# Performance work log

Hardware: AMD Instinct MI355X
Metric: run time of the kernel (lower is better)

Reference implementation:

```python
import jax, jax.numpy as jnp
import numpy as np

NUM_HEADS = 8
ALPHA = 4.0
BN_EPS = 1e-5


def _dwconv(x, w, pad):
    # x: [B, C, H, W], w: [C, 1, kh, kw] depthwise (groups == C)
    return jax.lax.conv_general_dilated(
        x, w, window_strides=(1, 1), padding=[(pad, pad), (pad, pad)],
        dimension_numbers=('NCHW', 'OIHW', 'NCHW'),
        feature_group_count=x.shape[1])


def _forward(x, qg_w, kv_w, proj_w, proj_b, dwc_w, dwc_b, power_p, scale_p,
             enh_w, bn_gamma, bn_beta, enhance_weight, pos_enc):
    B, N, C = x.shape
    H = W = int(round(N ** 0.5))
    h = NUM_HEADS
    d = C // h

    # qg linear (no bias): [B, N, 2C] -> q, g
    qg = jnp.einsum('bnc,oc->bno', x, qg_w)
    q, g = qg[..., :C], qg[..., C:]

    # SpatialFilterEnhancer on q: depthwise 3x3 conv + BN(train) + ReLU
    qi = q.transpose(0, 2, 1).reshape(B, C, H, W)
    qe = _dwconv(qi, enh_w, pad=1)
    m = qe.mean(axis=(0, 2, 3), keepdims=True)
    var = qe.var(axis=(0, 2, 3), keepdims=True)
    qe = (qe - m) * jax.lax.rsqrt(var + BN_EPS)
    qe = qe * bn_gamma[None, :, None, None] + bn_beta[None, :, None, None]
    qe = jax.nn.relu(qe)
    q_enh = qe.reshape(B, C, N).transpose(0, 2, 1)
    q = q + enhance_weight * q_enh

    # kv linear (sr_ratio == 1 path)
    kv = jnp.einsum('bnc,oc->bno', x, kv_w)
    k, v = kv[..., :C], kv[..., C:]
    k = k + pos_enc  # learned positional encoding, shape [1, N, C]
    n = k.shape[1]

    scale = jax.nn.softplus(scale_p)              # [1, 1, C]
    power = 1.0 + ALPHA * jax.nn.sigmoid(power_p)  # [1, h, 1, d]
    q = q / scale
    k = k / scale

    # split heads: [B, h, N, d]
    q = q.reshape(B, N, h, d).transpose(0, 2, 1, 3)
    k = k.reshape(B, n, h, d).transpose(0, 2, 1, 3)
    v = v.reshape(B, n, h, d).transpose(0, 2, 1, 3)

    # power-law kernel feature maps
    q_pos = jax.nn.relu(q) ** power
    q_neg = jax.nn.relu(-q) ** power
    k_pos = jax.nn.relu(k) ** power
    k_neg = jax.nn.relu(-k) ** power
    q_sim = jnp.concatenate([q_pos, q_neg], axis=-1)   # [B, h, N, 2d]
    q_opp = jnp.concatenate([q_neg, q_pos], axis=-1)
    kf = jnp.concatenate([k_pos, k_neg], axis=-1)      # [B, h, n, 2d]
    v1, v2 = jnp.split(v, 2, axis=-1)                  # [B, h, n, d/2] each

    k_mean = kf.mean(axis=-2)  # [B, h, 2d]
    inv_n = 1.0 / n

    # sim branch
    z = 1.0 / (jnp.einsum('bhnd,bhd->bhn', q_sim, k_mean)[..., None] + 1e-6)
    kv1 = jnp.einsum('bhnd,bhne->bhde', kf, v1) * inv_n  # (n^-0.5)*(n^-0.5)
    x_sim = jnp.einsum('bhnd,bhde->bhne', q_sim, kv1) * z

    # opp branch
    z2 = 1.0 / (jnp.einsum('bhnd,bhd->bhn', q_opp, k_mean)[..., None] + 1e-6)
    kv2 = jnp.einsum('bhnd,bhne->bhde', kf, v2) * inv_n
    x_opp = jnp.einsum('bhnd,bhde->bhne', q_opp, kv2) * z2

    xa = jnp.concatenate([x_sim, x_opp], axis=-1)       # [B, h, N, d]
    xa = xa.transpose(0, 2, 1, 3).reshape(B, N, C)

    # depthwise conv positional branch on v (sr_ratio == 1 -> no interpolate)
    vimg = v.reshape(B * h, H, W, d).transpose(0, 3, 1, 2)  # [B*h, d, H, W]
    vd = _dwconv(vimg, dwc_w, pad=2) + dwc_b[None, :, None, None]
    v_out = vd.reshape(B, C, N).transpose(0, 2, 1)          # [B, N, C]

    out = (xa + v_out) * g
    out = jnp.einsum('bnc,oc->bno', out, proj_w) + proj_b
    return out


def setup_inputs() -> dict:
    key = jax.random.key(0)
    ks = jax.random.split(key, 10)
    B, N, C = 8, 3136, 512
    h = NUM_HEADS
    d = C // h
    f = lambda k, shape, s=0.02: jax.random.normal(k, shape, jnp.float32) * s
    return dict(
        x=jax.random.normal(ks[0], (B, N, C), jnp.float32),
        qg_w=f(ks[1], (2 * C, C)),
        kv_w=f(ks[2], (2 * C, C)),
        proj_w=f(ks[3], (C, C)),
        proj_b=jnp.zeros((C,), jnp.float32),
        dwc_w=f(ks[4], (d, 1, 5, 5), 0.1),
        dwc_b=jnp.zeros((d,), jnp.float32),
        power_p=f(ks[5], (1, h, 1, d), 0.1),
        scale_p=f(ks[6], (1, 1, C), 0.1),
        enh_w=f(ks[7], (C, 1, 3, 3), 0.1),
        bn_gamma=jnp.ones((C,), jnp.float32),
        bn_beta=jnp.zeros((C,), jnp.float32),
        enhance_weight=jnp.float32(0.5),
        pos_enc=f(ks[8], (1, N, C)),
    )


def reference(x, qg_w, kv_w, proj_w, proj_b, dwc_w, dwc_b, power_p, scale_p,
              enh_w, bn_gamma, bn_beta, enhance_weight, pos_enc):
    return _forward(x, qg_w, kv_w, proj_w, proj_b, dwc_w, dwc_b, power_p,
                    scale_p, enh_w, bn_gamma, bn_beta, enhance_weight, pos_enc)
```

## Files before the change

### kernel.cpp

```cpp
#include <hip/hip_runtime.h>
#include <hip/hip_bf16.h>
#include <math.h>

#define CDIM 512
#define NTOK 3136
#define BATCH 8
#define MTOT (BATCH*NTOK)
#define NHEAD 8
#define DHEAD 64
#define HW 56

typedef __attribute__((ext_vector_type(8))) short short8;
typedef __attribute__((ext_vector_type(4))) float f32x4;

__device__ __forceinline__ ushort f2bf(float f) {
    union { float f; unsigned int u; } v; v.f = f;
    unsigned int u = v.u + 0x7FFFu + ((v.u >> 16) & 1u);
    return (ushort)(u >> 16);
}
__device__ __forceinline__ float bf2f(ushort u) {
    union { unsigned int u; float f; } v; v.u = ((unsigned int)u) << 16;
    return v.f;
}

__device__ __forceinline__ void gload_lds16(const void* g, void* lds) {
    __builtin_amdgcn_global_load_lds((const __attribute__((address_space(1))) void*)g,
                                     (__attribute__((address_space(3))) void*)lds,
                                     16, 0, 0);
}

__global__ void prep_kernel(const float* __restrict__ scale_p,
                            const float* __restrict__ power_p,
                            float* __restrict__ inv_scale,
                            float* __restrict__ power) {
    int c = threadIdx.x;
    if (c < CDIM) {
        float s = log1pf(expf(scale_p[c]));
        inv_scale[c] = 1.0f / s;
        power[c] = 1.0f + 4.0f / (1.0f + expf(-power_p[c]));
    }
}

__global__ __launch_bounds__(256) void cvt_bf16_kernel(const float* __restrict__ src,
                                                       ushort* __restrict__ dst, int n4) {
    int i = blockIdx.x * 256 + threadIdx.x;
    if (i < n4) {
        float4 f = ((const float4*)src)[i];
        ushort4 o;
        o.x = f2bf(f.x); o.y = f2bf(f.y); o.z = f2bf(f.z); o.w = f2bf(f.w);
        ((ushort4*)dst)[i] = o;
    }
}

__global__ __launch_bounds__(256) void mgemm_qgkv(const ushort* __restrict__ A,
                                                  const ushort* __restrict__ Wqg,
                                                  const ushort* __restrict__ Wkv,
                                                  ushort* __restrict__ Qout,
                                                  ushort* __restrict__ Gout,
                                                  ushort* __restrict__ KFout,
                                                  ushort* __restrict__ Vout,
                                                  const float* __restrict__ pos,
                                                  const float* __restrict__ invs,
                                                  const float* __restrict__ powr) {
    __shared__ __align__(16) char smem[65536];
    ushort* At = (ushort*)smem;
    ushort* Bt = (ushort*)(smem + 32768);
    float*  Osh = (float*)smem;

    const int t = threadIdx.x;
    const int w = t >> 6, l = t & 63;
    const int wr = w >> 1, wc = w & 1;
    const int r8 = l >> 3, sl = l & 7;
    const int ss = sl ^ r8;

    const int bid = blockIdx.x;
    const int idp = (bid & 7) * 392 + (bid >> 3);
    const int mb = idp >> 4, ob = idp & 15;
    const int m0 = mb * 128;
    const ushort* Bp = (ob < 8) ? (Wqg + (size_t)ob * 128 * CDIM)
                                : (Wkv + (size_t)(ob - 8) * 128 * CDIM);

    auto stage = [&](int buf, int ks) {
        const int k0 = ks * 64;
        #pragma unroll
        for (int c = 0; c < 4; ++c) {
            int rc = (w * 4 + c) * 8 + r8;
            gload_lds16(A + (size_t)(m0 + rc) * CDIM + k0 + ss * 8, At + buf * 8192 + (w * 4 + c) * 512);
            gload_lds16(Bp + (size_t)rc * CDIM + k0 + ss * 8, Bt + buf * 8192 + (w * 4 + c) * 512);
        }
    };

    f32x4 acc[4][4] = {};
    stage(0, 0);
    __syncthreads();
    for (int ks = 0; ks < 8; ++ks) {
        int cur = ks & 1;
        if (ks < 7) stage(cur ^ 1, ks + 1);
        #pragma unroll
        for (int kk = 0; kk < 2; ++kk) {
            short8 af[4], bfr[4];
            const int sbase = kk * 4 + (l >> 4);
            #pragma unroll
            for (int i = 0; i < 4; ++i) {
                int row = wr * 64 + i * 16 + (l & 15);
                af[i] = *(const short8*)&At[cur * 8192 + row * 64 + ((sbase ^ (row & 7)) * 8)];
                int rowb = wc * 64 + i * 16 + (l & 15);
                bfr[i] = *(const short8*)&Bt[cur * 8192 + rowb * 64 + ((sbase ^ (rowb & 7)) * 8)];
            }
            #pragma unroll
            for (int i = 0; i < 4; ++i)
                #pragma unroll
                for (int j = 0; j < 4; ++j)
                    acc[i][j] = __builtin_amdgcn_mfma_f32_16x16x32_bf16(af[i], bfr[j], acc[i][j], 0, 0, 0);
        }
        __syncthreads();
    }

    #pragma unroll
    for (int i = 0; i < 4; ++i)
        #pragma unroll
        for (int j = 0; j < 4; ++j)
            #pragma unroll
            for (int rr = 0; rr < 4; ++rr) {
                int row = wr * 64 + i * 16 + (l >> 4) * 4 + rr;
                int col = wc * 64 + j * 16 + (l & 15);
                int pc = col ^ (((row >> 2) & 1) << 4);
                Osh[row * 128 + pc] = acc[i][j][rr];
            }
    __syncthreads();

    const int colbase = ob * 128;
    #pragma unroll
    for (int q = 0; q < 16; ++q) {
        int fi = q * 256 + t;
        int r = fi >> 5, c4 = (fi & 31) * 4;
        int pc4 = c4 ^ (((r >> 2) & 1) << 4);
        float4 v = *(float4*)&Osh[r * 128 + pc4];
        int m = m0 + r;
        if (colbase < 512) {
            ushort4 o;
            o.x = f2bf(v.x); o.y = f2bf(v.y); o.z = f2bf(v.z); o.w = f2bf(v.w);
            *(ushort4*)&Qout[(size_t)m * CDIM + colbase + c4] = o;
        } else if (colbase < 1024) {
            ushort4 o;
            o.x = f2bf(v.x); o.y = f2bf(v.y); o.z = f2bf(v.z); o.w = f2bf(v.w);
            *(ushort4*)&Gout[(size_t)m * CDIM + colbase - 512 + c4] = o;
        } else if (colbase < 1536) {
            int n = m % NTOK;
            int oc = colbase - 1024 + c4;
            float4 pv = *(const float4*)&pos[(size_t)n * CDIM + oc];
            float4 iv = *(const float4*)&invs[oc];
            float4 pw = *(const float4*)&powr[oc];
            float kx0 = (v.x + pv.x) * iv.x, kx1 = (v.y + pv.y) * iv.y;
            float kx2 = (v.z + pv.z) * iv.z, kx3 = (v.w + pv.w) * iv.w;
            float t0 = __powf(fabsf(kx0), pw.x), t1 = __powf(fabsf(kx1), pw.y);
            float t2 = __powf(fabsf(kx2), pw.z), t3 = __powf(fabsf(kx3), pw.w);
            ushort4 up, un;
            up.x = kx0 > 0.f ? f2bf(t0) : 0; un.x = kx0 < 0.f ? f2bf(t0) : 0;
            up.y = kx1 > 0.f ? f2bf(t1) : 0; un.y = kx1 < 0.f ? f2bf(t1) : 0;
            up.z = kx2 > 0.f ? f2bf(t2) : 0; un.z = kx2 < 0.f ? f2bf(t2) : 0;
            up.w = kx3 > 0.f ? f2bf(t3) : 0; un.w = kx3 < 0.f ? f2bf(t3) : 0;
            ushort* dst = KFout + (size_t)m * 1024 + ((oc >> 6) << 7) + (oc & 63);
            *(ushort4*)dst = up;
            *(ushort4*)(dst + 64) = un;
        } else {
            ushort4 o;
            o.x = f2bf(v.x); o.y = f2bf(v.y); o.z = f2bf(v.z); o.w = f2bf(v.w);
            *(ushort4*)&Vout[(size_t)m * CDIM + colbase - 1536 + c4] = o;
        }
    }
}

__global__ __launch_bounds__(256) void mgemm_proj(const ushort* __restrict__ A,
                                                  const ushort* __restrict__ W,
                                                  float* __restrict__ out,
                                                  const float* __restrict__ pb) {
    __shared__ __align__(16) char smem[65536];
    ushort* At = (ushort*)smem;
    ushort* Bt = (ushort*)(smem + 32768);
    float*  Osh = (float*)smem;

    const int t = threadIdx.x;
    const int w = t >> 6, l = t & 63;
    const int wr = w >> 1, wc = w & 1;
    const int r8 = l >> 3, sl = l & 7;
    const int ss = sl ^ r8;

    const int bid = blockIdx.x;
    const int idp = (bid & 7) * 98 + (bid >> 3);
    const int mb = idp >> 2, ob = idp & 3;
    const int m0 = mb * 128;
    const ushort* Bp = W + (size_t)ob * 128 * CDIM;

    auto stage = [&](int buf, int ks) {
        const int k0 = ks * 64;
        #pragma unroll
        for (int c = 0; c < 4; ++c) {
            int rc = (w * 4 + c) * 8 + r8;
            gload_lds16(A + (size_t)(m0 + rc) * CDIM + k0 + ss * 8, At + buf * 8192 + (w * 4 + c) * 512);
            gload_lds16(Bp + (size_t)rc * CDIM + k0 + ss * 8, Bt + buf * 8192 + (w * 4 + c) * 512);
        }
    };

    f32x4 acc[4][4] = {};
    stage(0, 0);
    __syncthreads();
    for (int ks = 0; ks < 8; ++ks) {
        int cur = ks & 1;
        if (ks < 7) stage(cur ^ 1, ks + 1);
        #pragma unroll
        for (int kk = 0; kk < 2; ++kk) {
            short8 af[4], bfr[4];
            const int sbase = kk * 4 + (l >> 4);
            #pragma unroll
            for (int i = 0; i < 4; ++i) {
                int row = wr * 64 + i * 16 + (l & 15);
                af[i] = *(const short8*)&At[cur * 8192 + row * 64 + ((sbase ^ (row & 7)) * 8)];
                int rowb = wc * 64 + i * 16 + (l & 15);
                bfr[i] = *(const short8*)&Bt[cur * 8192 + rowb * 64 + ((sbase ^ (rowb & 7)) * 8)];
            }
            #pragma unroll
            for (int i = 0; i < 4; ++i)
                #pragma unroll
                for (int j = 0; j < 4; ++j)
                    acc[i][j] = __builtin_amdgcn_mfma_f32_16x16x32_bf16(af[i], bfr[j], acc[i][j], 0, 0, 0);
        }
        __syncthreads();
    }

    #pragma unroll
    for (int i = 0; i < 4; ++i)
        #pragma unroll
        for (int j = 0; j < 4; ++j)
            #pragma unroll
            for (int rr = 0; rr < 4; ++rr) {
                int row = wr * 64 + i * 16 + (l >> 4) * 4 + rr;
                int col = wc * 64 + j * 16 + (l & 15);
                int pc = col ^ (((row >> 2) & 1) << 4);
                Osh[row * 128 + pc] = acc[i][j][rr];
            }
    __syncthreads();

    const int colbase = ob * 128;
    #pragma unroll
    for (int q = 0; q < 16; ++q) {
        int fi = q * 256 + t;
        int r = fi >> 5, c4 = (fi & 31) * 4;
        int pc4 = c4 ^ (((r >> 2) & 1) << 4);
        float4 v = *(float4*)&Osh[r * 128 + pc4];
        float4 b4 = *(const float4*)&pb[colbase + c4];
        v.x += b4.x; v.y += b4.y; v.z += b4.z; v.w += b4.w;
        *(float4*)&out[(size_t)(m0 + r) * CDIM + colbase + c4] = v;
    }
}

__global__ __launch_bounds__(256) void conv3s_kernel(const ushort* __restrict__ Qbf,
                                                     const float* __restrict__ enh_w,
                                                     ushort* __restrict__ QEbf,
                                                     float* __restrict__ ssum,
                                                     float* __restrict__ ssq) {
    const int t = threadIdx.x;
    const int c0 = t * 2;
    const int xpos = blockIdx.x;
    const int byc = blockIdx.y;
    const int b = byc >> 2, yc = byc & 3;
    const int y0 = yc * 14;

    float wgt[9][2];
    #pragma unroll
    for (int tap = 0; tap < 9; ++tap) {
        wgt[tap][0] = enh_w[c0 * 9 + tap];
        wgt[tap][1] = enh_w[(c0 + 1) * 9 + tap];
    }
    const size_t base = (size_t)b * NTOK * CDIM + c0;

    float2 win[3][3];
    auto ldrow = [&](int yy, float2* dst) {
        #pragma unroll
        for (int dx = 0; dx < 3; ++dx) {
            int xx = xpos + dx - 1;
            bool ok = (yy >= 0 && yy < HW && xx >= 0 && xx < HW);
            if (ok) {
                ushort2 uv = *(const ushort2*)(Qbf + base + ((size_t)(yy * HW + xx) << 9));
                dst[dx] = make_float2(bf2f(uv.x), bf2f(uv.y));
            } else {
                dst[dx] = make_float2(0.f, 0.f);
            }
        }
    };
    ldrow(y0 - 1, win[0]);
    ldrow(y0,     win[1]);

    float s1a = 0.f, s2a = 0.f, s1b = 0.f, s2b = 0.f;
    #pragma unroll
    for (int i = 0; i < 14; ++i) {
        int y = y0 + i;
        ldrow(y + 1, win[(i + 2) % 3]);
        float a0 = 0.f, a1 = 0.f;
        #pragma unroll
        for (int dy = 0; dy < 3; ++dy) {
            float2* row = win[(i + dy) % 3];
            #pragma unroll
            for (int dx = 0; dx < 3; ++dx) {
                a0 = fmaf(row[dx].x, wgt[dy * 3 + dx][0], a0);
                a1 = fmaf(row[dx].y, wgt[dy * 3 + dx][1], a1);
            }
        }
        ushort2 o; o.x = f2bf(a0); o.y = f2bf(a1);
        *(ushort2*)(QEbf + base + ((size_t)(y * HW + xpos) << 9)) = o;
        s1a += a0; s2a += a0 * a0;
        s1b += a1; s2b += a1 * a1;
    }
    atomicAdd(&ssum[c0], s1a);     atomicAdd(&ssq[c0], s2a);
    atomicAdd(&ssum[c0 + 1], s1b); atomicAdd(&ssq[c0 + 1], s2b);
}

__global__ void bnprep_kernel(const float* __restrict__ ssum, const float* __restrict__ ssq,
                              const float* __restrict__ bn_g, const float* __restrict__ bn_b,
                              float* __restrict__ achan, float* __restrict__ bchan) {
    int c = threadIdx.x;
    if (c < CDIM) {
        const float invM = 1.0f / (float)MTOT;
        float mean = ssum[c] * invM;
        float var  = ssq[c] * invM - mean * mean;
        float a = bn_g[c] * rsqrtf(var + 1e-5f);
        achan[c] = a;
        bchan[c] = bn_b[c] - mean * a;
    }
}

__global__ __launch_bounds__(256) void kvred4_kernel(const ushort* __restrict__ KF,
                                                     const ushort* __restrict__ Vbf,
                                                     float* __restrict__ PKV) {
    const int bh = blockIdx.x, chunk = blockIdx.y;
    const int b = bh >> 3, head = bh & 7;
    const int t = threadIdx.x;
    const int w = t >> 6, l = t & 63;
    const int lr = l & 15;
    const int ns = (l >> 4) * 8;

    const int nbase = b * NTOK + chunk * 448;
    const ushort* kf0 = KF  + ((size_t)(nbase + ns)) * 1024 + head * 128 + (w * 32 + lr);
    const ushort* vb0 = Vbf + ((size_t)(nbase + ns)) * 512  + head * 64  + lr;

    short8 ones;
    #pragma unroll
    for (int j = 0; j < 8; ++j) ones[j] = (lr == 0) ? (short)0x3F80 : (short)0;

    f32x4 acc[2][5] = {};
    for (int tile = 0; tile < 14; ++tile) {
        union { uint u[4]; short8 s; } ua[2], ub[4];
        #pragma unroll
        for (int i = 0; i < 2; ++i) {
            #pragma unroll
            for (int j = 0; j < 4; ++j) {
                uint lo = kf0[i * 16 + (size_t)(2 * j) * 1024];
                uint hi = kf0[i * 16 + (size_t)(2 * j + 1) * 1024];
                ua[i].u[j] = lo | (hi << 16);
            }
        }
        #pragma unroll
        for (int j5 = 0; j5 < 4; ++j5) {
            #pragma unroll
            for (int j = 0; j < 4; ++j) {
                uint lo = vb0[j5 * 16 + (size_t)(2 * j) * 512];
                uint hi = vb0[j5 * 16 + (size_t)(2 * j + 1) * 512];
                ub[j5].u[j] = lo | (hi << 16);
            }
        }
        #pragma unroll
        for (int i = 0; i < 2; ++i) {
            #pragma unroll
            for (int j5 = 0; j5 < 4; ++j5)
                acc[i][j5] = __builtin_amdgcn_mfma_f32_16x16x32_bf16(ua[i].s, ub[j5].s, acc[i][j5], 0, 0, 0);
            acc[i][4] = __builtin_amdgcn_mfma_f32_16x16x32_bf16(ua[i].s, ones, acc[i][4], 0, 0, 0);
        }
        kf0 += (size_t)32 * 1024;
        vb0 += (size_t)32 * 512;
    }
    size_t base = ((size_t)(chunk * 64 + bh)) * 8320;
    #pragma unroll
    for (int i = 0; i < 2; ++i) {
        int d0 = w * 32 + i * 16 + (l >> 4) * 4;
        #pragma unroll
        for (int j = 0; j < 5; ++j) {
            int e = j * 16 + lr;
            if (j < 4 || e == 64)
                *(f32x4*)(PKV + base + (size_t)e * 128 + d0) = acc[i][j];
        }
    }
}

__global__ __launch_bounds__(256) void kvreduce2_kernel(const float* __restrict__ PKV,
                                                        ushort* __restrict__ kvTbf) {
    int gid = blockIdx.x * 256 + threadIdx.x;
    const float inv_n = 1.0f / (float)NTOK;
    int bh = gid / 10240;
    int r  = gid - bh * 10240;
    int row = r >> 7, dcol = r & 127;
    int dlog = (((dcol >> 3) ^ (row & 7)) << 3) | (dcol & 7);
    float s = 0.f;
    if (row < 64) {
        int dsel = (row >= 32) ? (dlog ^ 64) : dlog;
        #pragma unroll
        for (int c = 0; c < 7; ++c) s += PKV[(size_t)c * 532480 + (size_t)bh * 8320 + row * 128 + dsel];
    } else if (row < 66) {
        int dsel = (row == 65) ? (dlog ^ 64) : dlog;
        #pragma unroll
        for (int c = 0; c < 7; ++c) s += PKV[(size_t)c * 532480 + (size_t)bh * 8320 + 64 * 128 + dsel];
    }
    kvTbf[gid] = (row < 66) ? f2bf(s * inv_n) : (ushort)0;
}

__global__ __launch_bounds__(256) void attn_mfma_kernel(const ushort* __restrict__ Qbf,
                                                        const ushort* __restrict__ QEbf,
                                                        const ushort* __restrict__ kvTbf,
                                                        const float* __restrict__ power,
                                                        const float* __restrict__ achan,
                                                        const float* __restrict__ bchan,
                                                        const float* __restrict__ invs,
                                                        const float* __restrict__ ewp,
                                                        ushort* __restrict__ ATTbf) {
    __shared__ ushort QF[64 * 128];
    __shared__ ushort BT[80 * 128];
    const int bh = blockIdx.x, tb = blockIdx.y;
    const int b = bh >> 3, head = bh & 7;
    const int t = threadIdx.x;
    const int w = t >> 6, l = t & 63;

    #pragma unroll
    for (int i = 0; i < 5; ++i) {
        int f = i * 256 + t;
        gload_lds16(kvTbf + (size_t)bh * 10240 + f * 8, BT + f * 8);
    }

    const int c = l, hc = head * 64 + c;
    const float p = power[hc];
    const float ac = achan[hc], bc = bchan[hc], iv = invs[hc], ew = ewp[0];
    #pragma unroll
    for (int i = 0; i < 16; ++i) {
        int tok = i * 4 + w;
        size_t off = ((size_t)(b * NTOK + tb * 64 + tok)) * CDIM + hc;
        float q = bf2f(Qbf[off]);
        float qe = bf2f(QEbf[off]);
        q = (q + ew * fmaxf(fmaf(ac, qe, bc), 0.f)) * iv;
        float ax = fabsf(q);
        float tp = ax > 0.f ? __powf(ax, p) : 0.f;
        float qp = q > 0.f ? tp : 0.f;
        float qn = q < 0.f ? tp : 0.f;
        int sw = tok & 7;
        QF[tok * 128 + (((c >> 3) ^ sw) * 8) + (c & 7)]       = f2bf(qp);
        QF[tok * 128 + ((((c >> 3) + 8) ^ sw) * 8) + (c & 7)] = f2bf(qn);
    }
    __syncthreads();

    f32x4 acc[5] = {};
    #pragma unroll
    for (int kk = 0; kk < 4; ++kk) {
        int sbase = kk * 4 + (l >> 4);
        int rowa = w * 16 + (l & 15);
        short8 af = *(const short8*)&QF[rowa * 128 + ((sbase ^ (rowa & 7)) * 8)];
        #pragma unroll
        for (int j = 0; j < 5; ++j) {
            int rowb = j * 16 + (l & 15);
            short8 bf = *(const short8*)&BT[rowb * 128 + ((sbase ^ (rowb & 7)) * 8)];
            acc[j] = __builtin_amdgcn_mfma_f32_16x16x32_bf16(af, bf, acc[j], 0, 0, 0);
        }
    }
    __syncthreads();

    ushort* Oout = QF;
    #pragma unroll
    for (int rr = 0; rr < 4; ++rr) {
        float ssim = __shfl(acc[4][rr], (l & 48));
        float sopp = __shfl(acc[4][rr], (l & 48) + 1);
        float zs = 1.f / (ssim + 1e-6f);
        float zo = 1.f / (sopp + 1e-6f);
        int tokl = w * 16 + (l >> 4) * 4 + rr;
        #pragma unroll
        for (int j = 0; j < 4; ++j) {
            int e = j * 16 + (l & 15);
            Oout[tokl * 64 + e] = f2bf(acc[j][rr] * (j < 2 ? zs : zo));
        }
    }
    __syncthreads();

    #pragma unroll
    for (int i = 0; i < 2; ++i) {
        int idx = i * 256 + t;
        int tokl = idx >> 3, ch = (idx & 7) * 8;
        short8 vv = *(short8*)&Oout[tokl * 64 + ch];
        *(short8*)&ATTbf[((size_t)(b * NTOK + tb * 64 + tokl)) * CDIM + head * 64 + ch] = vv;
    }
}

__global__ __launch_bounds__(256) void voutg2_kernel(const ushort* __restrict__ Vbf,
                                                     const ushort* __restrict__ ATTbf,
                                                     const ushort* __restrict__ Gbf,
                                                     const float* __restrict__ dwc_w,
                                                     const float* __restrict__ dwc_b,
                                                     ushort* __restrict__ PRE) {
    const int t = threadIdx.x;
    const int c0 = t * 2;
    const int xpos = blockIdx.x;
    const int byc = blockIdx.y;
    const int b = byc >> 2, yc = byc & 3;
    const int y0 = yc * 14;
    const int dch = c0 & 63;

    float wgt[25][2];
    #pragma unroll
    for (int tap = 0; tap < 25; ++tap) {
        wgt[tap][0] = dwc_w[dch * 25 + tap];
        wgt[tap][1] = dwc_w[(dch + 1) * 25 + tap];
    }
    const float bias0 = dwc_b[dch], bias1 = dwc_b[dch + 1];
    const size_t base = (size_t)b * NTOK * CDIM + c0;

    float2 win[5][5];
    auto ldrow = [&](int yy, float2* dst) {
        #pragma unroll
        for (int dx = 0; dx < 5; ++dx) {
            int xx = xpos + dx - 2;
            bool ok = (yy >= 0 && yy < HW && xx >= 0 && xx < HW);
            if (ok) {
                ushort2 uv = *(const ushort2*)(Vbf + base + ((size_t)(yy * HW + xx) << 9));
                dst[dx] = make_float2(bf2f(uv.x), bf2f(uv.y));
            } else {
                dst[dx] = make_float2(0.f, 0.f);
            }
        }
    };
    ldrow(y0 - 2, win[0]);
    ldrow(y0 - 1, win[1]);
    ldrow(y0,     win[2]);
    ldrow(y0 + 1, win[3]);

    #pragma unroll
    for (int i = 0; i < 14; ++i) {
        int y = y0 + i;
        ldrow(y + 2, win[(i + 4) % 5]);
        float a0 = bias0, a1 = bias1;
        #pragma unroll
        for (int dy = 0; dy < 5; ++dy) {
            float2* row = win[(i + dy) % 5];
            #pragma unroll
            for (int dx = 0; dx < 5; ++dx) {
                a0 = fmaf(row[dx].x, wgt[dy * 5 + dx][0], a0);
                a1 = fmaf(row[dx].y, wgt[dy * 5 + dx][1], a1);
            }
        }
        size_t oidx = base + ((size_t)(y * HW + xpos) << 9);
        ushort2 au = *(const ushort2*)(ATTbf + oidx);
        ushort2 gu = *(const ushort2*)(Gbf + oidx);
        ushort2 o;
        o.x = f2bf((bf2f(au.x) + a0) * bf2f(gu.x));
        o.y = f2bf((bf2f(au.y) + a1) * bf2f(gu.y));
        *(ushort2*)(PRE + oidx) = o;
    }
}

extern "C" void kernel_launch(void* const* d_in, const int* in_sizes, int n_in,
                              void* d_out, int out_size, void* d_ws, size_t ws_size,
                              hipStream_t stream) {
    const float* x      = (const float*)d_in[0];
    const float* qg_w   = (const float*)d_in[1];
    const float* kv_w   = (const float*)d_in[2];
    const float* proj_w = (const float*)d_in[3];
    const float* proj_b = (const float*)d_in[4];
    const float* dwc_w  = (const float*)d_in[5];
    const float* dwc_b  = (const float*)d_in[6];
    const float* power_p= (const float*)d_in[7];
    const float* scale_p= (const float*)d_in[8];
    const float* enh_w  = (const float*)d_in[9];
    const float* bn_g   = (const float*)d_in[10];
    const float* bn_b   = (const float*)d_in[11];
    const float* ew_p   = (const float*)d_in[12];
    const float* pos    = (const float*)d_in[13];

    const size_t NELEM = (size_t)MTOT * CDIM;
    float* ws    = (float*)d_ws;
    ushort* Qbf  = (ushort*)ws;
    ushort* Gbf  = (ushort*)(ws + NELEM);
    float*  PKV  = ws + NELEM + NELEM / 2;
    ushort* KFbf = (ushort*)(ws + 2 * NELEM);
    ushort* PREbf= (ushort*)(ws + 2 * NELEM);
    ushort* Vbf  = (ushort*)(ws + 3 * NELEM);
    ushort* ATTbf= (ushort*)(ws + 3 * NELEM + NELEM / 2);
    ushort* Xbf  = (ushort*)(ws + 4 * NELEM);
    ushort* QEbf = (ushort*)(ws + 4 * NELEM);
    float* SMALL = ws + 5 * NELEM;
    float* ssum  = SMALL;
    float* ssq   = SMALL + 512;
    ushort* kvTbf= (ushort*)(SMALL + 9216);
    float* invs  = SMALL + 533504;
    float* powr  = SMALL + 534016;
    float* achan = SMALL + 534528;
    float* bchan = SMALL + 535040;
    ushort* Wqg  = (ushort*)(SMALL + 535552);
    ushort* Wkv  = (ushort*)(SMALL + 797696);
    ushort* Wproj= (ushort*)(SMALL + 1059840);

    hipMemsetAsync(SMALL, 0, (size_t)1024 * sizeof(float), stream);

    prep_kernel<<<1, 512, 0, stream>>>(scale_p, power_p, invs, powr);

    cvt_bf16_kernel<<<12544, 256, 0, stream>>>(x, Xbf, 3211264);
    cvt_bf16_kernel<<<512, 256, 0, stream>>>(qg_w, Wqg, 131072);
    cvt_bf16_kernel<<<512, 256, 0, stream>>>(kv_w, Wkv, 131072);
    cvt_bf16_kernel<<<256, 256, 0, stream>>>(proj_w, Wproj, 65536);

    mgemm_qgkv<<<3136, 256, 0, stream>>>(Xbf, Wqg, Wkv, Qbf, Gbf, KFbf, Vbf, pos, invs, powr);

    dim3 cgrid(56, 32);
    conv3s_kernel<<<cgrid, 256, 0, stream>>>(Qbf, enh_w, QEbf, ssum, ssq);
    bnprep_kernel<<<1, 512, 0, stream>>>(ssum, ssq, bn_g, bn_b, achan, bchan);

    kvred4_kernel<<<dim3(64, 7), 256, 0, stream>>>(KFbf, Vbf, PKV);
    kvreduce2_kernel<<<2560, 256, 0, stream>>>(PKV, kvTbf);

    attn_mfma_kernel<<<dim3(64, 49), 256, 0, stream>>>(Qbf, QEbf, kvTbf, powr,
                                                       achan, bchan, invs, ew_p, ATTbf);

    voutg2_kernel<<<cgrid, 256, 0, stream>>>(Vbf, ATTbf, Gbf, dwc_w, dwc_b, PREbf);

    mgemm_proj<<<784, 256, 0, stream>>>(PREbf, Wproj, (float*)d_out, proj_b);
}
```

Before: 502.2 us.

## Halve GEMM LDS by single-buffering tiles and staging epilogue in halves

Both bf16 GEMM kernels (qgkv and proj) drop from 64KB to 32KB of shared memory. The double-buffered K-stage pipeline becomes a single buffer with load-then-sync each step, and the output tile is written through LDS in two 64-row halves. The intent is to fit more workgroups per CU and raise occupancy. The cost is that global loads no longer overlap MFMA compute, and the epilogue gains extra barriers.

New measurement: 523.3 us. 1.04x slower.

```diff
diff --git a/kernel.cpp b/kernel.cpp
--- a/kernel.cpp
+++ b/kernel.cpp
@@ -62,9 +62,9 @@
                                                   const float* __restrict__ pos,
                                                   const float* __restrict__ invs,
                                                   const float* __restrict__ powr) {
-    __shared__ __align__(16) char smem[65536];
+    __shared__ __align__(16) char smem[32768];
     ushort* At = (ushort*)smem;
-    ushort* Bt = (ushort*)(smem + 32768);
+    ushort* Bt = (ushort*)(smem + 16384);
     float*  Osh = (float*)smem;
 
     const int t = threadIdx.x;
@@ -80,22 +80,20 @@
     const ushort* Bp = (ob < 8) ? (Wqg + (size_t)ob * 128 * CDIM)
                                 : (Wkv + (size_t)(ob - 8) * 128 * CDIM);
 
-    auto stage = [&](int buf, int ks) {
+    auto stage = [&](int ks) {
         const int k0 = ks * 64;
         #pragma unroll
         for (int c = 0; c < 4; ++c) {
             int rc = (w * 4 + c) * 8 + r8;
-            gload_lds16(A + (size_t)(m0 + rc) * CDIM + k0 + ss * 8, At + buf * 8192 + (w * 4 + c) * 512);
-            gload_lds16(Bp + (size_t)rc * CDIM + k0 + ss * 8, Bt + buf * 8192 + (w * 4 + c) * 512);
+            gload_lds16(A + (size_t)(m0 + rc) * CDIM + k0 + ss * 8, At + (w * 4 + c) * 512);
+            gload_lds16(Bp + (size_t)rc * CDIM + k0 + ss * 8, Bt + (w * 4 + c) * 512);
         }
     };
 
     f32x4 acc[4][4] = {};
-    stage(0, 0);
-    __syncthreads();
     for (int ks = 0; ks < 8; ++ks) {
-        int cur = ks & 1;
-        if (ks < 7) stage(cur ^ 1, ks + 1);
+        stage(ks);
+        __syncthreads();
         #pragma unroll
         for (int kk = 0; kk < 2; ++kk) {
             short8 af[4], bfr[4];
@@ -103,9 +101,9 @@
             #pragma unroll
             for (int i = 0; i < 4; ++i) {
                 int row = wr * 64 + i * 16 + (l & 15);
-                af[i] = *(const short8*)&At[cur * 8192 + row * 64 + ((sbase ^ (row & 7)) * 8)];
+                af[i] = *(const short8*)&At[row * 64 + ((sbase ^ (row & 7)) * 8)];
                 int rowb = wc * 64 + i * 16 + (l & 15);
-                bfr[i] = *(const short8*)&Bt[cur * 8192 + rowb * 64 + ((sbase ^ (rowb & 7)) * 8)];
+                bfr[i] = *(const short8*)&Bt[rowb * 64 + ((sbase ^ (rowb & 7)) * 8)];
             }
             #pragma unroll
             for (int i = 0; i < 4; ++i)
@@ -116,58 +114,63 @@
         __syncthreads();
     }
 
-    #pragma unroll
-    for (int i = 0; i < 4; ++i)
-        #pragma unroll
-        for (int j = 0; j < 4; ++j)
-            #pragma unroll
-            for (int rr = 0; rr < 4; ++rr) {
-                int row = wr * 64 + i * 16 + (l >> 4) * 4 + rr;
-                int col = wc * 64 + j * 16 + (l & 15);
-                int pc = col ^ (((row >> 2) & 1) << 4);
-                Osh[row * 128 + pc] = acc[i][j][rr];
-            }
-    __syncthreads();
-
     const int colbase = ob * 128;
     #pragma unroll
-    for (int q = 0; q < 16; ++q) {
-        int fi = q * 256 + t;
-        int r = fi >> 5, c4 = (fi & 31) * 4;
-        int pc4 = c4 ^ (((r >> 2) & 1) << 4);
-        float4 v = *(float4*)&Osh[r * 128 + pc4];
-        int m = m0 + r;
-        if (colbase < 512) {
-            ushort4 o;
-            o.x = f2bf(v.x); o.y = f2bf(v.y); o.z = f2bf(v.z); o.w = f2bf(v.w);
-            *(ushort4*)&Qout[(size_t)m * CDIM + colbase + c4] = o;
-        } else if (colbase < 1024) {
-            ushort4 o;
-            o.x = f2bf(v.x); o.y = f2bf(v.y); o.z = f2bf(v.z); o.w = f2bf(v.w);
-            *(ushort4*)&Gout[(size_t)m * CDIM + colbase - 512 + c4] = o;
-        } else if (colbase < 1536) {
-            int n = m % NTOK;
-            int oc = colbase - 1024 + c4;
-            float4 pv = *(const float4*)&pos[(size_t)n * CDIM + oc];
-            float4 iv = *(const float4*)&invs[oc];
-            float4 pw = *(const float4*)&powr[oc];
-            float kx0 = (v.x + pv.x) * iv.x, kx1 = (v.y + pv.y) * iv.y;
-            float kx2 = (v.z + pv.z) * iv.z, kx3 = (v.w + pv.w) * iv.w;
-            float t0 = __powf(fabsf(kx0), pw.x), t1 = __powf(fabsf(kx1), pw.y);
-            float t2 = __powf(fabsf(kx2), pw.z), t3 = __powf(fabsf(kx3), pw.w);
-            ushort4 up, un;
-            up.x = kx0 > 0.f ? f2bf(t0) : 0; un.x = kx0 < 0.f ? f2bf(t0) : 0;
-            up.y = kx1 > 0.f ? f2bf(t1) : 0; un.y = kx1 < 0.f ? f2bf(t1) : 0;
-            up.z = kx2 > 0.f ? f2bf(t2) : 0; un.z = kx2 < 0.f ? f2bf(t2) : 0;
-            up.w = kx3 > 0.f ? f2bf(t3) : 0; un.w = kx3 < 0.f ? f2bf(t3) : 0;
-            ushort* dst = KFout + (size_t)m * 1024 + ((oc >> 6) << 7) + (oc & 63);
-            *(ushort4*)dst = up;
-            *(ushort4*)(dst + 64) = un;
-        } else {
-            ushort4 o;
-            o.x = f2bf(v.x); o.y = f2bf(v.y); o.z = f2bf(v.z); o.w = f2bf(v.w);
-            *(ushort4*)&Vout[(size_t)m * CDIM + colbase - 1536 + c4] = o;
-        }
+    for (int p = 0; p < 2; ++p) {
+        if (wr == p) {
+            #pragma unroll
+            for (int i = 0; i < 4; ++i)
+                #pragma unroll
+                for (int j = 0; j < 4; ++j)
+                    #pragma unroll
+                    for (int rr = 0; rr < 4; ++rr) {
+                        int row = i * 16 + (l >> 4) * 4 + rr;
+                        int col = wc * 64 + j * 16 + (l & 15);
+                        int pc = col ^ (((row >> 2) & 1) << 4);
+                        Osh[row * 128 + pc] = acc[i][j][rr];
+                    }
+        }
+        __syncthreads();
+        #pragma unroll
+        for (int q = 0; q < 8; ++q) {
+            int fi = q * 256 + t;
+            int rl = fi >> 5, c4 = (fi & 31) * 4;
+            int pc4 = c4 ^ (((rl >> 2) & 1) << 4);
+            float4 v = *(float4*)&Osh[rl * 128 + pc4];
+            int m = m0 + p * 64 + rl;
+            if (colbase < 512) {
+                ushort4 o;
+                o.x = f2bf(v.x); o.y = f2bf(v.y); o.z = f2bf(v.z); o.w = f2bf(v.w);
+                *(ushort4*)&Qout[(size_t)m * CDIM + colbase + c4] = o;
+            } else if (colbase < 1024) {
+                ushort4 o;
+                o.x = f2bf(v.x); o.y = f2bf(v.y); o.z = f2bf(v.z); o.w = f2bf(v.w);
+                *(ushort4*)&Gout[(size_t)m * CDIM + colbase - 512 + c4] = o;
+            } else if (colbase < 1536) {
+                int n = m % NTOK;
+                int oc = colbase - 1024 + c4;
+                float4 pv = *(const float4*)&pos[(size_t)n * CDIM + oc];
+                float4 iv = *(const float4*)&invs[oc];
+                float4 pw = *(const float4*)&powr[oc];
+                float kx0 = (v.x + pv.x) * iv.x, kx1 = (v.y + pv.y) * iv.y;
+                float kx2 = (v.z + pv.z) * iv.z, kx3 = (v.w + pv.w) * iv.w;
+                float t0 = __powf(fabsf(kx0), pw.x), t1 = __powf(fabsf(kx1), pw.y);
+                float t2 = __powf(fabsf(kx2), pw.z), t3 = __powf(fabsf(kx3), pw.w);
+                ushort4 up, un;
+                up.x = kx0 > 0.f ? f2bf(t0) : 0; un.x = kx0 < 0.f ? f2bf(t0) : 0;
+                up.y = kx1 > 0.f ? f2bf(t1) : 0; un.y = kx1 < 0.f ? f2bf(t1) : 0;
+                up.z = kx2 > 0.f ? f2bf(t2) : 0; un.z = kx2 < 0.f ? f2bf(t2) : 0;
+                up.w = kx3 > 0.f ? f2bf(t3) : 0; un.w = kx3 < 0.f ? f2bf(t3) : 0;
+                ushort* dst = KFout + (size_t)m * 1024 + ((oc >> 6) << 7) + (oc & 63);
+                *(ushort4*)dst = up;
+                *(ushort4*)(dst + 64) = un;
+            } else {
+                ushort4 o;
+                o.x = f2bf(v.x); o.y = f2bf(v.y); o.z = f2bf(v.z); o.w = f2bf(v.w);
+                *(ushort4*)&Vout[(size_t)m * CDIM + colbase - 1536 + c4] = o;
+            }
+        }
+        __syncthreads();
     }
 }
 
@@ -175,9 +178,9 @@
                                                   const ushort* __restrict__ W,
                                                   float* __restrict__ out,
                                                   const float* __restrict__ pb) {
-    __shared__ __align__(16) char smem[65536];
+    __shared__ __align__(16) char smem[32768];
     ushort* At = (ushort*)smem;
-    ushort* Bt = (ushort*)(smem + 32768);
+    ushort* Bt = (ushort*)(smem + 16384);
     float*  Osh = (float*)smem;
 
     const int t = threadIdx.x;
@@ -192,22 +195,20 @@
     const int m0 = mb * 128;
     const ushort* Bp = W + (size_t)ob * 128 * CDIM;
 
-    auto stage = [&](int buf, int ks) {
+    auto stage = [&](int ks) {
         const int k0 = ks * 64;
         #pragma unroll
         for (int c = 0; c < 4; ++c) {
             int rc = (w * 4 + c) * 8 + r8;
-            gload_lds16(A + (size_t)(m0 + rc) * CDIM + k0 + ss * 8, At + buf * 8192 + (w * 4 + c) * 512);
-            gload_lds16(Bp + (size_t)rc * CDIM + k0 + ss * 8, Bt + buf * 8192 + (w * 4 + c) * 512);
+            gload_lds16(A + (size_t)(m0 + rc) * CDIM + k0 + ss * 8, At + (w * 4 + c) * 512);
+            gload_lds16(Bp + (size_t)rc * CDIM + k0 + ss * 8, Bt + (w * 4 + c) * 512);
         }
     };
 
     f32x4 acc[4][4] = {};
-    stage(0, 0);
-    __syncthreads();
     for (int ks = 0; ks < 8; ++ks) {
-        int cur = ks & 1;
-        if (ks < 7) stage(cur ^ 1, ks + 1);
+        stage(ks);
+        __syncthreads();
         #pragma unroll
         for (int kk = 0; kk < 2; ++kk) {
             short8 af[4], bfr[4];
@@ -215,9 +216,9 @@
             #pragma unroll
             for (int i = 0; i < 4; ++i) {
                 int row = wr * 64 + i * 16 + (l & 15);
-                af[i] = *(const short8*)&At[cur * 8192 + row * 64 + ((sbase ^ (row & 7)) * 8)];
+                af[i] = *(const short8*)&At[row * 64 + ((sbase ^ (row & 7)) * 8)];
                 int rowb = wc * 64 + i * 16 + (l & 15);
-                bfr[i] = *(const short8*)&Bt[cur * 8192 + rowb * 64 + ((sbase ^ (rowb & 7)) * 8)];
+                bfr[i] = *(const short8*)&Bt[rowb * 64 + ((sbase ^ (rowb & 7)) * 8)];
             }
             #pragma unroll
             for (int i = 0; i < 4; ++i)
@@ -228,29 +229,34 @@
         __syncthreads();
     }
 
-    #pragma unroll
-    for (int i = 0; i < 4; ++i)
-        #pragma unroll
-        for (int j = 0; j < 4; ++j)
-            #pragma unroll
-            for (int rr = 0; rr < 4; ++rr) {
-                int row = wr * 64 + i * 16 + (l >> 4) * 4 + rr;
-                int col = wc * 64 + j * 16 + (l & 15);
-                int pc = col ^ (((row >> 2) & 1) << 4);
-                Osh[row * 128 + pc] = acc[i][j][rr];
-            }
-    __syncthreads();
-
     const int colbase = ob * 128;
     #pragma unroll
-    for (int q = 0; q < 16; ++q) {
-        int fi = q * 256 + t;
-        int r = fi >> 5, c4 = (fi & 31) * 4;
-        int pc4 = c4 ^ (((r >> 2) & 1) << 4);
-        float4 v = *(float4*)&Osh[r * 128 + pc4];
-        float4 b4 = *(const float4*)&pb[colbase + c4];
-        v.x += b4.x; v.y += b4.y; v.z += b4.z; v.w += b4.w;
-        *(float4*)&out[(size_t)(m0 + r) * CDIM + colbase + c4] = v;
+    for (int p = 0; p < 2; ++p) {
+        if (wr == p) {
+            #pragma unroll
+            for (int i = 0; i < 4; ++i)
+                #pragma unroll
+                for (int j = 0; j < 4; ++j)
+                    #pragma unroll
+                    for (int rr = 0; rr < 4; ++rr) {
+                        int row = i * 16 + (l >> 4) * 4 + rr;
+                        int col = wc * 64 + j * 16 + (l & 15);
+                        int pc = col ^ (((row >> 2) & 1) << 4);
+                        Osh[row * 128 + pc] = acc[i][j][rr];
+                    }
+        }
+        __syncthreads();
+        #pragma unroll
+        for (int q = 0; q < 8; ++q) {
+            int fi = q * 256 + t;
+            int rl = fi >> 5, c4 = (fi & 31) * 4;
+            int pc4 = c4 ^ (((rl >> 2) & 1) << 4);
+            float4 v = *(float4*)&Osh[rl * 128 + pc4];
+            float4 b4 = *(const float4*)&pb[colbase + c4];
+            v.x += b4.x; v.y += b4.y; v.z += b4.z; v.w += b4.w;
+            *(float4*)&out[(size_t)(m0 + p * 64 + rl) * CDIM + colbase + c4] = v;
+        }
+        __syncthreads();
     }
 }
 
```

## Enlarge QGKV GEMM tile to 256 rows with 512-thread blocks and fuse weight casts

Applied to the files above, without the earlier changes.

The fused QG/KV projection GEMM now computes 256x128 output tiles with 8 waves per block instead of 128x128 with 4 waves. Each weight tile loaded into LDS is reused across twice as many rows, which cuts global B-operand traffic and halves the block count. The epilogue drains the accumulators through shared memory in two halves so the 64KB staging buffer still fits, at the cost of an extra barrier per half. The three separate weight-conversion launches are merged into one kernel to save launch overhead. LDS use rises to 96KB per block, which may limit occupancy.

Result: slower. 519.4 us (+3.4%).

```diff
diff --git a/kernel.cpp b/kernel.cpp
--- a/kernel.cpp
+++ b/kernel.cpp
@@ -52,7 +52,24 @@
     }
 }
 
-__global__ __launch_bounds__(256) void mgemm_qgkv(const ushort* __restrict__ A,
+__global__ __launch_bounds__(256) void cvt_weights_kernel(const float* __restrict__ qg_w,
+                                                          const float* __restrict__ kv_w,
+                                                          const float* __restrict__ proj_w,
+                                                          ushort* __restrict__ Wqg,
+                                                          ushort* __restrict__ Wkv,
+                                                          ushort* __restrict__ Wproj) {
+    int i = blockIdx.x * 256 + threadIdx.x;
+    const float* src; ushort* dst; int idx;
+    if (i < 131072)      { src = qg_w;   dst = Wqg;   idx = i; }
+    else if (i < 262144) { src = kv_w;   dst = Wkv;   idx = i - 131072; }
+    else                 { src = proj_w; dst = Wproj; idx = i - 262144; }
+    float4 f = ((const float4*)src)[idx];
+    ushort4 o;
+    o.x = f2bf(f.x); o.y = f2bf(f.y); o.z = f2bf(f.z); o.w = f2bf(f.w);
+    ((ushort4*)dst)[idx] = o;
+}
+
+__global__ __launch_bounds__(512) void mgemm_qgkv(const ushort* __restrict__ A,
                                                   const ushort* __restrict__ Wqg,
                                                   const ushort* __restrict__ Wkv,
                                                   ushort* __restrict__ Qout,
@@ -62,31 +79,37 @@
                                                   const float* __restrict__ pos,
                                                   const float* __restrict__ invs,
                                                   const float* __restrict__ powr) {
-    __shared__ __align__(16) char smem[65536];
+    __shared__ __align__(16) char smem[98304];
     ushort* At = (ushort*)smem;
-    ushort* Bt = (ushort*)(smem + 32768);
+    ushort* Bt = (ushort*)(smem + 65536);
     float*  Osh = (float*)smem;
 
     const int t = threadIdx.x;
     const int w = t >> 6, l = t & 63;
     const int wr = w >> 1, wc = w & 1;
-    const int r8 = l >> 3, sl = l & 7;
-    const int ss = sl ^ r8;
 
     const int bid = blockIdx.x;
-    const int idp = (bid & 7) * 392 + (bid >> 3);
+    const int idp = (bid & 7) * 196 + (bid >> 3);
     const int mb = idp >> 4, ob = idp & 15;
-    const int m0 = mb * 128;
+    const int m0 = mb * 256;
     const ushort* Bp = (ob < 8) ? (Wqg + (size_t)ob * 128 * CDIM)
                                 : (Wkv + (size_t)(ob - 8) * 128 * CDIM);
 
     auto stage = [&](int buf, int ks) {
         const int k0 = ks * 64;
         #pragma unroll
-        for (int c = 0; c < 4; ++c) {
-            int rc = (w * 4 + c) * 8 + r8;
-            gload_lds16(A + (size_t)(m0 + rc) * CDIM + k0 + ss * 8, At + buf * 8192 + (w * 4 + c) * 512);
-            gload_lds16(Bp + (size_t)rc * CDIM + k0 + ss * 8, Bt + buf * 8192 + (w * 4 + c) * 512);
+        for (int i = 0; i < 4; ++i) {
+            int f = t + i * 512;
+            int row = f >> 3, ps = f & 7;
+            int ls = ps ^ (row & 7);
+            gload_lds16(A + (size_t)(m0 + row) * CDIM + k0 + ls * 8, At + buf * 16384 + f * 8);
+        }
+        #pragma unroll
+        for (int i = 0; i < 2; ++i) {
+            int f = t + i * 512;
+            int row = f >> 3, ps = f & 7;
+            int ls = ps ^ (row & 7);
+            gload_lds16(Bp + (size_t)row * CDIM + k0 + ls * 8, Bt + buf * 8192 + f * 8);
         }
     };
 
@@ -103,7 +126,7 @@
             #pragma unroll
             for (int i = 0; i < 4; ++i) {
                 int row = wr * 64 + i * 16 + (l & 15);
-                af[i] = *(const short8*)&At[cur * 8192 + row * 64 + ((sbase ^ (row & 7)) * 8)];
+                af[i] = *(const short8*)&At[cur * 16384 + row * 64 + ((sbase ^ (row & 7)) * 8)];
                 int rowb = wc * 64 + i * 16 + (l & 15);
                 bfr[i] = *(const short8*)&Bt[cur * 8192 + rowb * 64 + ((sbase ^ (rowb & 7)) * 8)];
             }
@@ -116,58 +139,63 @@
         __syncthreads();
     }
 
-    #pragma unroll
-    for (int i = 0; i < 4; ++i)
-        #pragma unroll
-        for (int j = 0; j < 4; ++j)
-            #pragma unroll
-            for (int rr = 0; rr < 4; ++rr) {
-                int row = wr * 64 + i * 16 + (l >> 4) * 4 + rr;
-                int col = wc * 64 + j * 16 + (l & 15);
-                int pc = col ^ (((row >> 2) & 1) << 4);
-                Osh[row * 128 + pc] = acc[i][j][rr];
-            }
-    __syncthreads();
-
     const int colbase = ob * 128;
     #pragma unroll
-    for (int q = 0; q < 16; ++q) {
-        int fi = q * 256 + t;
-        int r = fi >> 5, c4 = (fi & 31) * 4;
-        int pc4 = c4 ^ (((r >> 2) & 1) << 4);
-        float4 v = *(float4*)&Osh[r * 128 + pc4];
-        int m = m0 + r;
-        if (colbase < 512) {
-            ushort4 o;
-            o.x = f2bf(v.x); o.y = f2bf(v.y); o.z = f2bf(v.z); o.w = f2bf(v.w);
-            *(ushort4*)&Qout[(size_t)m * CDIM + colbase + c4] = o;
-        } else if (colbase < 1024) {
-            ushort4 o;
-            o.x = f2bf(v.x); o.y = f2bf(v.y); o.z = f2bf(v.z); o.w = f2bf(v.w);
-            *(ushort4*)&Gout[(size_t)m * CDIM + colbase - 512 + c4] = o;
-        } else if (colbase < 1536) {
-            int n = m % NTOK;
-            int oc = colbase - 1024 + c4;
-            float4 pv = *(const float4*)&pos[(size_t)n * CDIM + oc];
-            float4 iv = *(const float4*)&invs[oc];
-            float4 pw = *(const float4*)&powr[oc];
-            float kx0 = (v.x + pv.x) * iv.x, kx1 = (v.y + pv.y) * iv.y;
-            float kx2 = (v.z + pv.z) * iv.z, kx3 = (v.w + pv.w) * iv.w;
-            float t0 = __powf(fabsf(kx0), pw.x), t1 = __powf(fabsf(kx1), pw.y);
-            float t2 = __powf(fabsf(kx2), pw.z), t3 = __powf(fabsf(kx3), pw.w);
-            ushort4 up, un;
-            up.x = kx0 > 0.f ? f2bf(t0) : 0; un.x = kx0 < 0.f ? f2bf(t0) : 0;
-            up.y = kx1 > 0.f ? f2bf(t1) : 0; un.y = kx1 < 0.f ? f2bf(t1) : 0;
-            up.z = kx2 > 0.f ? f2bf(t2) : 0; un.z = kx2 < 0.f ? f2bf(t2) : 0;
-            up.w = kx3 > 0.f ? f2bf(t3) : 0; un.w = kx3 < 0.f ? f2bf(t3) : 0;
-            ushort* dst = KFout + (size_t)m * 1024 + ((oc >> 6) << 7) + (oc & 63);
-            *(ushort4*)dst = up;
-            *(ushort4*)(dst + 64) = un;
-        } else {
-            ushort4 o;
-            o.x = f2bf(v.x); o.y = f2bf(v.y); o.z = f2bf(v.z); o.w = f2bf(v.w);
-            *(ushort4*)&Vout[(size_t)m * CDIM + colbase - 1536 + c4] = o;
-        }
+    for (int p = 0; p < 2; ++p) {
+        if ((wr >> 1) == p) {
+            #pragma unroll
+            for (int i = 0; i < 4; ++i)
+                #pragma unroll
+                for (int j = 0; j < 4; ++j)
+                    #pragma unroll
+                    for (int rr = 0; rr < 4; ++rr) {
+                        int rloc = (wr & 1) * 64 + i * 16 + (l >> 4) * 4 + rr;
+                        int col = wc * 64 + j * 16 + (l & 15);
+                        int pc = col ^ (((rloc >> 2) & 1) << 4);
+                        Osh[rloc * 128 + pc] = acc[i][j][rr];
+                    }
+        }
+        __syncthreads();
+        #pragma unroll
+        for (int q = 0; q < 8; ++q) {
+            int fi = q * 512 + t;
+            int r = fi >> 5, c4 = (fi & 31) * 4;
+            int pc4 = c4 ^ (((r >> 2) & 1) << 4);
+            float4 v = *(float4*)&Osh[r * 128 + pc4];
+            int m = m0 + p * 128 + r;
+            if (colbase < 512) {
+                ushort4 o;
+                o.x = f2bf(v.x); o.y = f2bf(v.y); o.z = f2bf(v.z); o.w = f2bf(v.w);
+                *(ushort4*)&Qout[(size_t)m * CDIM + colbase + c4] = o;
+            } else if (colbase < 1024) {
+                ushort4 o;
+                o.x = f2bf(v.x); o.y = f2bf(v.y); o.z = f2bf(v.z); o.w = f2bf(v.w);
+                *(ushort4*)&Gout[(size_t)m * CDIM + colbase - 512 + c4] = o;
+            } else if (colbase < 1536) {
+                int n = m % NTOK;
+                int oc = colbase - 1024 + c4;
+                float4 pv = *(const float4*)&pos[(size_t)n * CDIM + oc];
+                float4 iv = *(const float4*)&invs[oc];
+                float4 pw = *(const float4*)&powr[oc];
+                float kx0 = (v.x + pv.x) * iv.x, kx1 = (v.y + pv.y) * iv.y;
+                float kx2 = (v.z + pv.z) * iv.z, kx3 = (v.w + pv.w) * iv.w;
+                float t0 = __powf(fabsf(kx0), pw.x), t1 = __powf(fabsf(kx1), pw.y);
+                float t2 = __powf(fabsf(kx2), pw.z), t3 = __powf(fabsf(kx3), pw.w);
+                ushort4 up, un;
+                up.x = kx0 > 0.f ? f2bf(t0) : 0; un.x = kx0 < 0.f ? f2bf(t0) : 0;
+                up.y = kx1 > 0.f ? f2bf(t1) : 0; un.y = kx1 < 0.f ? f2bf(t1) : 0;
+                up.z = kx2 > 0.f ? f2bf(t2) : 0; un.z = kx2 < 0.f ? f2bf(t2) : 0;
+                up.w = kx3 > 0.f ? f2bf(t3) : 0; un.w = kx3 < 0.f ? f2bf(t3) : 0;
+                ushort* dst = KFout + (size_t)m * 1024 + ((oc >> 6) << 7) + (oc & 63);
+                *(ushort4*)dst = up;
+                *(ushort4*)(dst + 64) = un;
+            } else {
+                ushort4 o;
+                o.x = f2bf(v.x); o.y = f2bf(v.y); o.z = f2bf(v.z); o.w = f2bf(v.w);
+                *(ushort4*)&Vout[(size_t)m * CDIM + colbase - 1536 + c4] = o;
+            }
+        }
+        __syncthreads();
     }
 }
 
@@ -606,11 +634,9 @@
     prep_kernel<<<1, 512, 0, stream>>>(scale_p, power_p, invs, powr);
 
     cvt_bf16_kernel<<<12544, 256, 0, stream>>>(x, Xbf, 3211264);
-    cvt_bf16_kernel<<<512, 256, 0, stream>>>(qg_w, Wqg, 131072);
-    cvt_bf16_kernel<<<512, 256, 0, stream>>>(kv_w, Wkv, 131072);
-    cvt_bf16_kernel<<<256, 256, 0, stream>>>(proj_w, Wproj, 65536);
-
-    mgemm_qgkv<<<3136, 256, 0, stream>>>(Xbf, Wqg, Wkv, Qbf, Gbf, KFbf, Vbf, pos, invs, powr);
+    cvt_weights_kernel<<<1280, 256, 0, stream>>>(qg_w, kv_w, proj_w, Wqg, Wkv, Wproj);
+
+    mgemm_qgkv<<<1568, 512, 0, stream>>>(Xbf, Wqg, Wkv, Qbf, Gbf, KFbf, Vbf, pos, invs, powr);
 
     dim3 cgrid(56, 32);
     conv3s_kernel<<<cgrid, 256, 0, stream>>>(Qbf, enh_w, QEbf, ssum, ssq);
```

## Triple-buffer GEMM k-loop with vmcnt waits and merge weight conversions

Applied to the files above, without the earlier changes.

Both bf16 MFMA GEMM kernels move from double to triple-buffered LDS staging, growing shared memory from 64KB to 96KB. Explicit s_waitcnt vmcnt plus a single barrier per iteration replace the two __syncthreads, so two stages of global-to-LDS loads stay in flight while compute runs. The three weight-conversion launches are merged into one kernel to cut launch overhead. The larger LDS footprint may lower occupancy, and the vmcnt(8) count has to match the exact number of outstanding loads per stage.

New measurement: 541.1 us. 7.8% more time.

```diff
diff --git a/kernel.cpp b/kernel.cpp
--- a/kernel.cpp
+++ b/kernel.cpp
@@ -50,6 +50,23 @@
         o.x = f2bf(f.x); o.y = f2bf(f.y); o.z = f2bf(f.z); o.w = f2bf(f.w);
         ((ushort4*)dst)[i] = o;
     }
+}
+
+__global__ __launch_bounds__(256) void cvt_weights_kernel(const float* __restrict__ qg_w,
+                                                          const float* __restrict__ kv_w,
+                                                          const float* __restrict__ proj_w,
+                                                          ushort* __restrict__ Wqg,
+                                                          ushort* __restrict__ Wkv,
+                                                          ushort* __restrict__ Wproj) {
+    int i = blockIdx.x * 256 + threadIdx.x;
+    const float* src; ushort* dst; int idx;
+    if (i < 131072)      { src = qg_w;   dst = Wqg;   idx = i; }
+    else if (i < 262144) { src = kv_w;   dst = Wkv;   idx = i - 131072; }
+    else                 { src = proj_w; dst = Wproj; idx = i - 262144; }
+    float4 f = ((const float4*)src)[idx];
+    ushort4 o;
+    o.x = f2bf(f.x); o.y = f2bf(f.y); o.z = f2bf(f.z); o.w = f2bf(f.w);
+    ((ushort4*)dst)[idx] = o;
 }
 
 __global__ __launch_bounds__(256) void mgemm_qgkv(const ushort* __restrict__ A,
@@ -62,9 +79,9 @@
                                                   const float* __restrict__ pos,
                                                   const float* __restrict__ invs,
                                                   const float* __restrict__ powr) {
-    __shared__ __align__(16) char smem[65536];
+    __shared__ __align__(16) char smem[98304];
     ushort* At = (ushort*)smem;
-    ushort* Bt = (ushort*)(smem + 32768);
+    ushort* Bt = (ushort*)(smem + 49152);
     float*  Osh = (float*)smem;
 
     const int t = threadIdx.x;
@@ -92,10 +109,13 @@
 
     f32x4 acc[4][4] = {};
     stage(0, 0);
-    __syncthreads();
+    stage(1, 1);
     for (int ks = 0; ks < 8; ++ks) {
-        int cur = ks & 1;
-        if (ks < 7) stage(cur ^ 1, ks + 1);
+        if (ks < 7) asm volatile("s_waitcnt vmcnt(8)" ::: "memory");
+        else        asm volatile("s_waitcnt vmcnt(0)" ::: "memory");
+        __builtin_amdgcn_s_barrier();
+        if (ks + 2 < 8) stage((ks + 2) % 3, ks + 2);
+        const int cur = ks % 3;
         #pragma unroll
         for (int kk = 0; kk < 2; ++kk) {
             short8 af[4], bfr[4];
@@ -113,8 +133,8 @@
                 for (int j = 0; j < 4; ++j)
                     acc[i][j] = __builtin_amdgcn_mfma_f32_16x16x32_bf16(af[i], bfr[j], acc[i][j], 0, 0, 0);
         }
-        __syncthreads();
-    }
+    }
+    __syncthreads();
 
     #pragma unroll
     for (int i = 0; i < 4; ++i)
@@ -175,9 +195,9 @@
                                                   const ushort* __restrict__ W,
                                                   float* __restrict__ out,
                                                   const float* __restrict__ pb) {
-    __shared__ __align__(16) char smem[65536];
+    __shared__ __align__(16) char smem[98304];
     ushort* At = (ushort*)smem;
-    ushort* Bt = (ushort*)(smem + 32768);
+    ushort* Bt = (ushort*)(smem + 49152);
     float*  Osh = (float*)smem;
 
     const int t = threadIdx.x;
@@ -204,10 +224,13 @@
 
     f32x4 acc[4][4] = {};
     stage(0, 0);
-    __syncthreads();
+    stage(1, 1);
     for (int ks = 0; ks < 8; ++ks) {
-        int cur = ks & 1;
-        if (ks < 7) stage(cur ^ 1, ks + 1);
+        if (ks < 7) asm volatile("s_waitcnt vmcnt(8)" ::: "memory");
+        else        asm volatile("s_waitcnt vmcnt(0)" ::: "memory");
+        __builtin_amdgcn_s_barrier();
+        if (ks + 2 < 8) stage((ks + 2) % 3, ks + 2);
+        const int cur = ks % 3;
         #pragma unroll
         for (int kk = 0; kk < 2; ++kk) {
             short8 af[4], bfr[4];
@@ -225,8 +248,8 @@
                 for (int j = 0; j < 4; ++j)
                     acc[i][j] = __builtin_amdgcn_mfma_f32_16x16x32_bf16(af[i], bfr[j], acc[i][j], 0, 0, 0);
         }
-        __syncthreads();
-    }
+    }
+    __syncthreads();
 
     #pragma unroll
     for (int i = 0; i < 4; ++i)
@@ -606,9 +629,7 @@
     prep_kernel<<<1, 512, 0, stream>>>(scale_p, power_p, invs, powr);
 
     cvt_bf16_kernel<<<12544, 256, 0, stream>>>(x, Xbf, 3211264);
-    cvt_bf16_kernel<<<512, 256, 0, stream>>>(qg_w, Wqg, 131072);
-    cvt_bf16_kernel<<<512, 256, 0, stream>>>(kv_w, Wkv, 131072);
-    cvt_bf16_kernel<<<256, 256, 0, stream>>>(proj_w, Wproj, 65536);
+    cvt_weights_kernel<<<1280, 256, 0, stream>>>(qg_w, kv_w, proj_w, Wqg, Wkv, Wproj);
 
     mgemm_qgkv<<<3136, 256, 0, stream>>>(Xbf, Wqg, Wkv, Qbf, Gbf, KFbf, Vbf, pos, invs, powr);
 
```
